# Kernel optimization log

Hardware: AMD Instinct MI355X
Metric: run time of the kernel (lower is better)

Reference implementation:

```python
import jax, jax.numpy as jnp
import numpy as np

WS = 8      # window_size
NH = 6      # num_heads
SHIFT = 4   # shift_size


def setup_inputs() -> dict:
    key = jax.random.key(0)
    k0, k1, k2, k3, k4 = jax.random.split(key, 5)
    B, C, H, W = 4, 192, 224, 224
    x = jax.random.normal(k0, (B, C, H, W), jnp.float32)
    # 1x1 convs == per-pixel linear layers: store weights as (out, in)
    w_qkv = jax.random.normal(k1, (3 * C, C), jnp.float32) * 0.05
    b_qkv = jax.random.normal(k2, (3 * C,), jnp.float32) * 0.05
    w_proj = jax.random.normal(k3, (C, C), jnp.float32) * 0.05
    b_proj = jax.random.normal(k4, (C,), jnp.float32) * 0.05
    return {"x": x, "w_qkv": w_qkv, "b_qkv": b_qkv, "w_proj": w_proj, "b_proj": b_proj}


def reference(x, w_qkv, b_qkv, w_proj, b_proj):
    B, C, H, W = x.shape
    hd = C // NH
    scale = hd ** -0.5

    if SHIFT > 0:
        x = jnp.roll(x, shift=(-SHIFT, -SHIFT), axis=(2, 3))

    pad_r = (WS - W % WS) % WS
    pad_b = (WS - H % WS) % WS
    if pad_r > 0 or pad_b > 0:
        x = jnp.pad(x, ((0, 0), (0, 0), (0, pad_b), (0, pad_r)))
    Hp, Wp = x.shape[2], x.shape[3]
    Hn, Wn = Hp // WS, Wp // WS

    # qkv 1x1 conv: (B,C,Hp,Wp) -> (B,3C,Hp,Wp)
    qkv = jnp.einsum('bchw,oc->bohw', x, w_qkv) + b_qkv[None, :, None, None]

    # (B,3,NH,hd,Hn,WS,Wn,WS) -> (3,B,Hn,Wn,NH,WS,WS,hd)
    qkv = qkv.reshape(B, 3, NH, hd, Hn, WS, Wn, WS)
    qkv = jnp.transpose(qkv, (1, 0, 4, 6, 2, 5, 7, 3))
    q = qkv[0].reshape(-1, NH, WS * WS, hd)  # (B*Hn*Wn, NH, 64, hd)
    k = qkv[1].reshape(-1, NH, WS * WS, hd)
    v = qkv[2].reshape(-1, NH, WS * WS, hd)

    attn = jax.nn.softmax(jnp.einsum('wnqd,wnkd->wnqk', q, k) * scale, axis=-1)
    out = jnp.einsum('wnqk,wnkd->wnqd', attn, v)

    # (B,Hn,Wn,NH,WS,WS,hd) -> (B,NH,hd,Hn,WS,Wn,WS) -> (B,C,Hp,Wp)
    out = out.reshape(B, Hn, Wn, NH, WS, WS, hd)
    out = jnp.transpose(out, (0, 3, 6, 1, 4, 2, 5)).reshape(B, C, Hp, Wp)

    out = jnp.einsum('bchw,oc->bohw', out, w_proj) + b_proj[None, :, None, None]

    if pad_r > 0 or pad_b > 0:
        out = out[:, :, :H, :W]
    if SHIFT > 0:
        out = jnp.roll(out, shift=(SHIFT, SHIFT), axis=(2, 3))
    return out
```

## Files before the change

### kernel.cpp

```cpp
#include <hip/hip_runtime.h>
#include <stdint.h>

#define HHW   224
#define CCH   192
#define SHIFT 4
#define NWIN  3136
#define NTOK  200704
#define QN    38535168ull

typedef __attribute__((ext_vector_type(8))) short bf16x8;
typedef __attribute__((ext_vector_type(4))) float f32x4;

__device__ __forceinline__ ushort f2bf(float f) {
    union { float f; uint32_t i; } v; v.f = f;
    uint32_t u = v.i;
    return (ushort)((u + 0x7FFFu + ((u >> 16) & 1u)) >> 16);
}
__device__ __forceinline__ uint32_t pk2(float a, float b) {
    return (uint32_t)f2bf(a) | ((uint32_t)f2bf(b) << 16);
}

__global__ __launch_bounds__(256) void prep_w(const float* __restrict__ w,
                                              ushort* __restrict__ wo, int nrow)
{
    int idx = blockIdx.x * 256 + threadIdx.x;
    if (idx >= nrow * 24) return;
    int rg = idx / 24, p = idx % 24;
    int s = p ^ (rg & 7);
    const float* src = w + (size_t)rg * 192 + s * 8;
    float4 a = *(const float4*)src;
    float4 b = *(const float4*)(src + 4);
    uint4 o;
    o.x = pk2(a.x, a.y); o.y = pk2(a.z, a.w);
    o.z = pk2(b.x, b.y); o.w = pk2(b.z, b.w);
    *(uint4*)(wo + (size_t)rg * 192 + p * 8) = o;
}

__global__ __launch_bounds__(256) void prep_x(const float* __restrict__ x,
                                              ushort* __restrict__ xo)
{
    __shared__ ushort lt[1792 * 8];
    const int blk = blockIdx.x;
    const int oct = blk % 24;
    const int bh  = blk / 24;
    const int hn  = bh % 28;
    const float* xb = x + ((size_t)(bh / 28) * CCH + oct * 8) * (HHW * HHW);

    for (int u = threadIdx.x; u < 448; u += 256) {
        int r = u / 56, q = u % 56;
        int hh = (hn * 8 + r + SHIFT) % HHW;
        int ww = (q * 4 + SHIFT) % HHW;
        const float* src = xb + (size_t)hh * HHW + ww;
        float4 v[8];
        #pragma unroll
        for (int c = 0; c < 8; c++)
            v[c] = *(const float4*)(src + (size_t)c * (HHW * HHW));
        #pragma unroll
        for (int i = 0; i < 4; i++) {
            int p = u * 4 + i;
            int sw = p ^ ((p >> 3) & 7);
            uint4 o;
            o.x = pk2(((const float*)&v[0])[i], ((const float*)&v[1])[i]);
            o.y = pk2(((const float*)&v[2])[i], ((const float*)&v[3])[i]);
            o.z = pk2(((const float*)&v[4])[i], ((const float*)&v[5])[i]);
            o.w = pk2(((const float*)&v[6])[i], ((const float*)&v[7])[i]);
            *(uint4*)&lt[sw * 8] = o;
        }
    }
    __syncthreads();

    for (int u = threadIdx.x; u < 1792; u += 256) {
        int wn = u >> 6, t = u & 63;
        int p = (t >> 3) * 224 + wn * 8 + (t & 7);
        int sw = p ^ ((p >> 3) & 7);
        *(uint4*)(xo + (size_t)(bh * 28 + wn) * 12288 + oct * 512 + t * 8) =
            *(const uint4*)&lt[sw * 8];
    }
}

template<int OCH>
__global__ __launch_bounds__(256, 3) void gemm_win(
    const ushort* __restrict__ xin, const ushort* __restrict__ wbf,
    const float* __restrict__ bias,
    ushort* __restrict__ qo, ushort* __restrict__ ko, ushort* __restrict__ vto,
    float* __restrict__ dout)
{
    __shared__ ushort wc[96 * 192];

    const int tid = threadIdx.x;
    const int wave = tid >> 6, lane = tid & 63;
    const int quad = lane >> 4, l16 = lane & 15;
    const int p0 = blockIdx.x * 128 + wave * 32;

    #pragma unroll
    for (int it = 0; it < 9; it++) {
        int off = (it * 4 + wave) * 512;
        __builtin_amdgcn_global_load_lds(
            (const __attribute__((address_space(1))) void*)(wbf + off + lane * 8),
            (__attribute__((address_space(3))) void*)(&wc[off]), 16, 0, 0);
    }

    bf16x8 bfr[2][6];
    #pragma unroll
    for (int nt = 0; nt < 2; nt++) {
        int token = p0 + nt * 16 + l16;
        #pragma unroll
        for (int k = 0; k < 6; k++) {
            if (OCH == 576)
                bfr[nt][k] = *(const bf16x8*)(xin + (size_t)(token >> 6) * 12288
                                              + (k * 4 + quad) * 512 + (token & 63) * 8);
            else
                bfr[nt][k] = *(const bf16x8*)(xin + (size_t)token * CCH + k * 32 + quad * 8);
        }
    }

    __syncthreads();

    #pragma unroll
    for (int ch = 0; ch < OCH / 96; ch++) {
        f32x4 acc[6][2];
        #pragma unroll
        for (int m = 0; m < 6; m++)
            #pragma unroll
            for (int nt = 0; nt < 2; nt++) acc[m][nt] = (f32x4){0.f, 0.f, 0.f, 0.f};

        const ushort* wl = wc + (size_t)l16 * 192;
        #pragma unroll
        for (int k = 0; k < 6; k++) {
            const ushort* wk = wl + ((k * 4 + quad) ^ (l16 & 7)) * 8;
            #pragma unroll
            for (int m = 0; m < 6; m++) {
                bf16x8 afrag = *(const bf16x8*)(wk + m * 3072);
                acc[m][0] = __builtin_amdgcn_mfma_f32_16x16x32_bf16(afrag, bfr[0][k], acc[m][0], 0, 0, 0);
                acc[m][1] = __builtin_amdgcn_mfma_f32_16x16x32_bf16(afrag, bfr[1][k], acc[m][1], 0, 0, 0);
            }
        }

        if (ch + 1 < OCH / 96) {
            __syncthreads();
            const ushort* wsrc = wbf + (size_t)(ch + 1) * (96 * 192);
            #pragma unroll
            for (int it = 0; it < 9; it++) {
                int off = (it * 4 + wave) * 512;
                __builtin_amdgcn_global_load_lds(
                    (const __attribute__((address_space(1))) void*)(wsrc + off + lane * 8),
                    (__attribute__((address_space(3))) void*)(&wc[off]), 16, 0, 0);
            }
        }

        const int obase = ch * 96;
        #pragma unroll
        for (int m = 0; m < 6; m++) {
            const int o0 = obase + m * 16 + quad * 4;
            float4 bb = *(const float4*)(bias + o0);
            #pragma unroll
            for (int nt = 0; nt < 2; nt++) {
                int token = p0 + nt * 16 + l16;
                int win = token >> 6, t = token & 63;
                float f0 = acc[m][nt][0] + bb.x, f1 = acc[m][nt][1] + bb.y;
                float f2 = acc[m][nt][2] + bb.z, f3 = acc[m][nt][3] + bb.w;
                if (OCH == 576) {
                    const int s = o0 / 192;
                    const int rem = o0 % 192;
                    const int h = rem >> 5, d0 = rem & 31;
                    size_t wh = (size_t)win * 6 + h;
                    if (s == 2) {
                        vto[(wh * 32 + d0 + 0) * 64 + t] = f2bf(f0);
                        vto[(wh * 32 + d0 + 1) * 64 + t] = f2bf(f1);
                        vto[(wh * 32 + d0 + 2) * 64 + t] = f2bf(f2);
                        vto[(wh * 32 + d0 + 3) * 64 + t] = f2bf(f3);
                    } else {
                        uint2 pk;
                        pk.x = pk2(f0, f1);
                        pk.y = pk2(f2, f3);
                        ushort* dst = (s == 0 ? qo : ko) + (wh * 64 + t) * 32 + d0;
                        *(uint2*)dst = pk;
                    }
                } else {
                    int b = win / 784, hn = (win / 28) % 28, wn = win % 28;
                    int hh = (hn * 8 + (t >> 3) + SHIFT) % HHW;
                    int ww = (wn * 8 + (t & 7) + SHIFT) % HHW;
                    float* dst = dout + ((size_t)(b * CCH + o0) * HHW + hh) * HHW + ww;
                    dst[0] = f0; dst[(size_t)HHW * HHW] = f1;
                    dst[2 * (size_t)HHW * HHW] = f2; dst[3 * (size_t)HHW * HHW] = f3;
                }
            }
        }
        if (ch + 1 < OCH / 96) __syncthreads();
    }
}

__global__ __launch_bounds__(384, 3) void attn_win(
    ushort* qx2,
    const ushort* __restrict__ k, const ushort* __restrict__ vt)
{
    __shared__ ushort pt[6][64][72];

    const int tid = threadIdx.x;
    const int h = tid >> 6, lane = tid & 63;
    const int quad = lane >> 4, l16 = lane & 15;
    const int win = blockIdx.x;

    const ushort* qp = qx2 + (size_t)(win * 6 + h) * 2048;
    const ushort* kp = k   + (size_t)(win * 6 + h) * 2048;
    const ushort* vp = vt  + (size_t)(win * 6 + h) * 2048;

    bf16x8 kf[4], vf[2][2];
    #pragma unroll
    for (int nt = 0; nt < 4; nt++) kf[nt] = *(const bf16x8*)&kp[(nt * 16 + l16) * 32 + quad * 8];
    #pragma unroll
    for (int ks = 0; ks < 2; ks++)
        #pragma unroll
        for (int nt = 0; nt < 2; nt++)
            vf[ks][nt] = *(const bf16x8*)&vp[(nt * 16 + l16) * 64 + ks * 32 + quad * 8];

    f32x4 s[4][4];
    #pragma unroll
    for (int mt = 0; mt < 4; mt++) {
        bf16x8 qf = *(const bf16x8*)&qp[(mt * 16 + l16) * 32 + quad * 8];
        #pragma unroll
        for (int nt = 0; nt < 4; nt++) {
            s[mt][nt] = (f32x4){0.f, 0.f, 0.f, 0.f};
            s[mt][nt] = __builtin_amdgcn_mfma_f32_16x16x32_bf16(qf, kf[nt], s[mt][nt], 0, 0, 0);
        }
    }

    const float SC = 0.25506953149031837f;
    #pragma unroll
    for (int mt = 0; mt < 4; mt++) {
        #pragma unroll
        for (int rg = 0; rg < 4; rg++) {
            float v0 = s[mt][0][rg], v1 = s[mt][1][rg], v2 = s[mt][2][rg], v3 = s[mt][3][rg];
            float mx = fmaxf(fmaxf(v0, v1), fmaxf(v2, v3));
            #pragma unroll
            for (int msk = 1; msk < 16; msk <<= 1) mx = fmaxf(mx, __shfl_xor(mx, msk, 64));
            float e0 = exp2f((v0 - mx) * SC), e1 = exp2f((v1 - mx) * SC);
            float e2 = exp2f((v2 - mx) * SC), e3 = exp2f((v3 - mx) * SC);
            float sm = (e0 + e1) + (e2 + e3);
            #pragma unroll
            for (int msk = 1; msk < 16; msk <<= 1) sm += __shfl_xor(sm, msk, 64);
            float r = __builtin_amdgcn_rcpf(sm);
            int qt = mt * 16 + quad * 4 + rg;
            pt[h][qt][ 0 + l16] = f2bf(e0 * r);
            pt[h][qt][16 + l16] = f2bf(e1 * r);
            pt[h][qt][32 + l16] = f2bf(e2 * r);
            pt[h][qt][48 + l16] = f2bf(e3 * r);
        }
    }
    __syncthreads();

    f32x4 o[4][2];
    #pragma unroll
    for (int mt = 0; mt < 4; mt++)
        #pragma unroll
        for (int nt = 0; nt < 2; nt++) o[mt][nt] = (f32x4){0.f, 0.f, 0.f, 0.f};
    #pragma unroll
    for (int ks = 0; ks < 2; ks++)
        #pragma unroll
        for (int mt = 0; mt < 4; mt++) {
            bf16x8 pf = *(const bf16x8*)&pt[h][mt * 16 + l16][ks * 32 + quad * 8];
            #pragma unroll
            for (int nt = 0; nt < 2; nt++)
                o[mt][nt] = __builtin_amdgcn_mfma_f32_16x16x32_bf16(pf, vf[ks][nt], o[mt][nt], 0, 0, 0);
        }

    ushort* x2 = qx2 + (size_t)win * 12288;
    #pragma unroll
    for (int mt = 0; mt < 4; mt++)
        #pragma unroll
        for (int nt = 0; nt < 2; nt++)
            #pragma unroll
            for (int rg = 0; rg < 4; rg++) {
                int qt = mt * 16 + quad * 4 + rg;
                x2[qt * CCH + h * 32 + nt * 16 + l16] = f2bf(o[mt][nt][rg]);
            }
}

extern "C" void kernel_launch(void* const* d_in, const int* in_sizes, int n_in,
                              void* d_out, int out_size, void* d_ws, size_t ws_size,
                              hipStream_t stream) {
    const float* x      = (const float*)d_in[0];
    const float* w_qkv  = (const float*)d_in[1];
    const float* b_qkv  = (const float*)d_in[2];
    const float* w_proj = (const float*)d_in[3];
    const float* b_proj = (const float*)d_in[4];
    float* out = (float*)d_out;
    ushort* ws = (ushort*)d_ws;

    ushort* X1 = (ushort*)d_out;
    ushort* WQ = (ushort*)d_out + QN;
    ushort* Q  = ws;
    ushort* K  = ws + QN;
    ushort* VT = ws + 2 * QN;
    ushort* WP = VT;

    prep_w       <<<54, 256, 0, stream>>>(w_qkv, WQ, 576);
    prep_x       <<<4 * 28 * 24, 256, 0, stream>>>(x, X1);
    gemm_win<576><<<NTOK / 128, 256, 0, stream>>>(X1, WQ, b_qkv, Q, K, VT, nullptr);
    attn_win     <<<NWIN, 384, 0, stream>>>(Q, K, VT);
    prep_w       <<<18, 256, 0, stream>>>(w_proj, WP, 192);
    gemm_win<192><<<NTOK / 128, 256, 0, stream>>>(Q, WP, b_proj, nullptr, nullptr, nullptr, out);
}
```

Measured before the change: 564.8 us.

## Transpose attention MFMAs so softmax reduces in-lane with swizzled LDS

Computes S^T = K·Q^T instead of Q·K^T so each lane holds a whole column of scores for one query, cutting the softmax reductions from four cross-lane shuffle steps per row to two. The probability tile moves to an XOR-swizzled unpadded LDS layout written with packed 8-byte stores, and the output is computed as V^T·P^T so results are written as packed 4-element bf16 stores instead of scalar stores. Launch bounds are raised to allow 4 blocks per CU, which may force register spilling or tighter allocation.

After: 514.2 us. 8.9% less time.

```diff
diff --git a/kernel.cpp b/kernel.cpp
--- a/kernel.cpp
+++ b/kernel.cpp
@@ -190,11 +190,11 @@
     }
 }
 
-__global__ __launch_bounds__(384, 3) void attn_win(
+__global__ __launch_bounds__(384, 4) void attn_win(
     ushort* qx2,
     const ushort* __restrict__ k, const ushort* __restrict__ vt)
 {
-    __shared__ ushort pt[6][64][72];
+    __shared__ ushort pt[6][64 * 64];
 
     const int tid = threadIdx.x;
     const int h = tid >> 6, lane = tid & 63;
@@ -205,75 +205,94 @@
     const ushort* kp = k   + (size_t)(win * 6 + h) * 2048;
     const ushort* vp = vt  + (size_t)(win * 6 + h) * 2048;
 
-    bf16x8 kf[4], vf[2][2];
+    bf16x8 kf[4], qf[4], vf[2][2];
     #pragma unroll
     for (int nt = 0; nt < 4; nt++) kf[nt] = *(const bf16x8*)&kp[(nt * 16 + l16) * 32 + quad * 8];
     #pragma unroll
+    for (int nt = 0; nt < 4; nt++) qf[nt] = *(const bf16x8*)&qp[(nt * 16 + l16) * 32 + quad * 8];
+    #pragma unroll
+    for (int md = 0; md < 2; md++)
+        #pragma unroll
+        for (int ks = 0; ks < 2; ks++)
+            vf[md][ks] = *(const bf16x8*)&vp[(md * 16 + l16) * 64 + ks * 32 + quad * 8];
+
+    const float SC = 0.25506953149031837f;
+    ushort* ph = pt[h];
+
+    #pragma unroll
+    for (int nq = 0; nq < 4; nq += 2) {
+        f32x4 sc[2][4];
+        #pragma unroll
+        for (int j = 0; j < 2; j++)
+            #pragma unroll
+            for (int mk = 0; mk < 4; mk++) {
+                sc[j][mk] = (f32x4){0.f, 0.f, 0.f, 0.f};
+                sc[j][mk] = __builtin_amdgcn_mfma_f32_16x16x32_bf16(kf[mk], qf[nq + j], sc[j][mk], 0, 0, 0);
+            }
+        #pragma unroll
+        for (int j = 0; j < 2; j++) {
+            float mx = sc[j][0][0];
+            #pragma unroll
+            for (int mk = 0; mk < 4; mk++)
+                #pragma unroll
+                for (int rg = 0; rg < 4; rg++) mx = fmaxf(mx, sc[j][mk][rg]);
+            mx = fmaxf(mx, __shfl_xor(mx, 16, 64));
+            mx = fmaxf(mx, __shfl_xor(mx, 32, 64));
+            float e[4][4];
+            float sm = 0.f;
+            #pragma unroll
+            for (int mk = 0; mk < 4; mk++)
+                #pragma unroll
+                for (int rg = 0; rg < 4; rg++) {
+                    e[mk][rg] = exp2f((sc[j][mk][rg] - mx) * SC);
+                    sm += e[mk][rg];
+                }
+            sm += __shfl_xor(sm, 16, 64);
+            sm += __shfl_xor(sm, 32, 64);
+            float r = __builtin_amdgcn_rcpf(sm);
+            const int q = (nq + j) * 16 + l16;
+            const int sx = q & 7;
+            ushort* row = ph + q * 64;
+            #pragma unroll
+            for (int mk = 0; mk < 4; mk++) {
+                uint2 w;
+                w.x = pk2(e[mk][0] * r, e[mk][1] * r);
+                w.y = pk2(e[mk][2] * r, e[mk][3] * r);
+                int s0 = mk * 2 + (quad >> 1);
+                *(uint2*)(row + (((s0 ^ sx) << 3) + (quad & 1) * 4)) = w;
+            }
+        }
+    }
+    __syncthreads();
+
+    f32x4 o[2][4];
+    #pragma unroll
+    for (int md = 0; md < 2; md++)
+        #pragma unroll
+        for (int nq = 0; nq < 4; nq++) o[md][nq] = (f32x4){0.f, 0.f, 0.f, 0.f};
+    #pragma unroll
     for (int ks = 0; ks < 2; ks++)
         #pragma unroll
-        for (int nt = 0; nt < 2; nt++)
-            vf[ks][nt] = *(const bf16x8*)&vp[(nt * 16 + l16) * 64 + ks * 32 + quad * 8];
-
-    f32x4 s[4][4];
-    #pragma unroll
-    for (int mt = 0; mt < 4; mt++) {
-        bf16x8 qf = *(const bf16x8*)&qp[(mt * 16 + l16) * 32 + quad * 8];
-        #pragma unroll
-        for (int nt = 0; nt < 4; nt++) {
-            s[mt][nt] = (f32x4){0.f, 0.f, 0.f, 0.f};
-            s[mt][nt] = __builtin_amdgcn_mfma_f32_16x16x32_bf16(qf, kf[nt], s[mt][nt], 0, 0, 0);
-        }
-    }
-
-    const float SC = 0.25506953149031837f;
-    #pragma unroll
-    for (int mt = 0; mt < 4; mt++) {
-        #pragma unroll
-        for (int rg = 0; rg < 4; rg++) {
-            float v0 = s[mt][0][rg], v1 = s[mt][1][rg], v2 = s[mt][2][rg], v3 = s[mt][3][rg];
-            float mx = fmaxf(fmaxf(v0, v1), fmaxf(v2, v3));
-            #pragma unroll
-            for (int msk = 1; msk < 16; msk <<= 1) mx = fmaxf(mx, __shfl_xor(mx, msk, 64));
-            float e0 = exp2f((v0 - mx) * SC), e1 = exp2f((v1 - mx) * SC);
-            float e2 = exp2f((v2 - mx) * SC), e3 = exp2f((v3 - mx) * SC);
-            float sm = (e0 + e1) + (e2 + e3);
-            #pragma unroll
-            for (int msk = 1; msk < 16; msk <<= 1) sm += __shfl_xor(sm, msk, 64);
-            float r = __builtin_amdgcn_rcpf(sm);
-            int qt = mt * 16 + quad * 4 + rg;
-            pt[h][qt][ 0 + l16] = f2bf(e0 * r);
-            pt[h][qt][16 + l16] = f2bf(e1 * r);
-            pt[h][qt][32 + l16] = f2bf(e2 * r);
-            pt[h][qt][48 + l16] = f2bf(e3 * r);
-        }
-    }
-    __syncthreads();
-
-    f32x4 o[4][2];
-    #pragma unroll
-    for (int mt = 0; mt < 4; mt++)
-        #pragma unroll
-        for (int nt = 0; nt < 2; nt++) o[mt][nt] = (f32x4){0.f, 0.f, 0.f, 0.f};
-    #pragma unroll
-    for (int ks = 0; ks < 2; ks++)
-        #pragma unroll
-        for (int mt = 0; mt < 4; mt++) {
-            bf16x8 pf = *(const bf16x8*)&pt[h][mt * 16 + l16][ks * 32 + quad * 8];
-            #pragma unroll
-            for (int nt = 0; nt < 2; nt++)
-                o[mt][nt] = __builtin_amdgcn_mfma_f32_16x16x32_bf16(pf, vf[ks][nt], o[mt][nt], 0, 0, 0);
+        for (int nq = 0; nq < 4; nq++) {
+            const int q = nq * 16 + l16;
+            bf16x8 pf = *(const bf16x8*)(ph + q * 64 + ((((ks * 4 + quad) ^ (q & 7))) << 3));
+            #pragma unroll
+            for (int md = 0; md < 2; md++)
+                o[md][nq] = __builtin_amdgcn_mfma_f32_16x16x32_bf16(vf[md][ks], pf, o[md][nq], 0, 0, 0);
         }
 
     ushort* x2 = qx2 + (size_t)win * 12288;
     #pragma unroll
-    for (int mt = 0; mt < 4; mt++)
-        #pragma unroll
-        for (int nt = 0; nt < 2; nt++)
-            #pragma unroll
-            for (int rg = 0; rg < 4; rg++) {
-                int qt = mt * 16 + quad * 4 + rg;
-                x2[qt * CCH + h * 32 + nt * 16 + l16] = f2bf(o[mt][nt][rg]);
-            }
+    for (int md = 0; md < 2; md++)
+        #pragma unroll
+        for (int nq = 0; nq < 4; nq++) {
+            const int q = nq * 16 + l16;
+            const int c = h * 32 + md * 16 + quad * 4;
+            uint2 w;
+            w.x = pk2(o[md][nq][0], o[md][nq][1]);
+            w.y = pk2(o[md][nq][2], o[md][nq][3]);
+            *(uint2*)(x2 + q * CCH + c) = w;
+        }
 }
 
 extern "C" void kernel_launch(void* const* d_in, const int* in_sizes, int n_in,
```
